# Kernel optimization log

Measured on AMD Instinct MI355X. Metric: run time of the kernel, lower is better.

The kernel has to match this reference:

```python
import jax, jax.numpy as jnp
import numpy as np
import math

B, S, D, H = 2, 4096, 512, 8
DK = D // H


def setup_inputs() -> dict:
    key = jax.random.key(0)
    ks = jax.random.split(key, 9)
    s = 1.0 / math.sqrt(D)
    return {
        "x": jax.random.normal(ks[0], (B, S, D), dtype=jnp.float32),
        "Wq": jax.random.normal(ks[1], (D, D), dtype=jnp.float32) * s,
        "bq": jax.random.normal(ks[2], (D,), dtype=jnp.float32) * 0.01,
        "Wk": jax.random.normal(ks[3], (D, D), dtype=jnp.float32) * s,
        "bk": jax.random.normal(ks[4], (D,), dtype=jnp.float32) * 0.01,
        "Wv": jax.random.normal(ks[5], (D, D), dtype=jnp.float32) * s,
        "bv": jax.random.normal(ks[6], (D,), dtype=jnp.float32) * 0.01,
        "Wo": jax.random.normal(ks[7], (D, D), dtype=jnp.float32) * s,
        "bo": jax.random.normal(ks[8], (D,), dtype=jnp.float32) * 0.01,
    }


def reference(x, Wq, bq, Wk, bk, Wv, bv, Wo, bo):
    b, s, _ = x.shape
    # projections, split into heads: (b, h, s, dk)
    def proj(W, bias):
        return (x @ W.T + bias).reshape(b, s, H, DK).transpose(0, 2, 1, 3)
    Q, K, V = proj(Wq, bq), proj(Wk, bk), proj(Wv, bv)
    scale = 1.0 / math.sqrt(DK)
    scores = jnp.einsum("bhqd,bhkd->bhqk", Q, K) * scale  # (b,h,s,s)
    causal = jnp.tril(jnp.ones((s, s), dtype=bool))
    scores = jnp.where(causal[None, None], scores, -jnp.inf)
    attn = jax.nn.softmax(scores, axis=-1)
    out = jnp.einsum("bhqk,bhkd->bhqd", attn, V)
    out = out.transpose(0, 2, 1, 3).reshape(b, s, D)
    return out @ Wo.T + bo
```

## Files before the change

kernel.cpp:

```cpp
#include <hip/hip_runtime.h>
#include <hip/hip_bf16.h>

using u16    = unsigned short;
using u32    = unsigned int;
using bf16x8 = __attribute__((ext_vector_type(8))) __bf16;
using s16x4  = __attribute__((ext_vector_type(4))) short;
using f32x4  = __attribute__((ext_vector_type(4))) float;
using u16x4  = __attribute__((ext_vector_type(4))) unsigned short;
using u16x8  = __attribute__((ext_vector_type(8))) unsigned short;
using u32x2  = __attribute__((ext_vector_type(2))) unsigned int;
using u32x4  = __attribute__((ext_vector_type(4))) unsigned int;


static __device__ __forceinline__ u16 f2bf(float f) {
  unsigned int u = __float_as_uint(f);
  u += 0x7fffu + ((u >> 16) & 1u);
  return (u16)(u >> 16);
}
static __device__ __forceinline__ u32 pack2bf(float lo, float hi) {
  return __builtin_amdgcn_perm(__float_as_uint(hi), __float_as_uint(lo), 0x07060302u);
}

__global__ __launch_bounds__(256) void cvt_all(
    const float* __restrict__ x,  const float* __restrict__ wq,
    const float* __restrict__ wk, const float* __restrict__ wv,
    const float* __restrict__ wo,
    u16* __restrict__ xb, u16* __restrict__ wqb, u16* __restrict__ wkb,
    u16* __restrict__ wvb, u16* __restrict__ wob) {
  const int bx = blockIdx.x;
  const float* src;
  u16* dst;
  int i;
  if (bx < 4096) {
    src = x; dst = xb; i = bx * 256 + threadIdx.x;
  } else {
    const int t  = (bx - 4096) >> 8;
    const int lb = (bx - 4096) & 255;
    src = (t == 0) ? wq : (t == 1) ? wk : (t == 2) ? wv : wo;
    dst = (t == 0) ? wqb : (t == 1) ? wkb : (t == 2) ? wvb : wob;
    i = lb * 256 + threadIdx.x;
  }
  float4 v = reinterpret_cast<const float4*>(src)[i];
  u16x4 o = { f2bf(v.x), f2bf(v.y), f2bf(v.z), f2bf(v.w) };
  reinterpret_cast<u16x4*>(dst)[i] = o;
}

__global__ __launch_bounds__(256, 3) void gemm_qkv(const u16* __restrict__ A,
                                                   const u16* __restrict__ Wq,
                                                   const u16* __restrict__ Wk,
                                                   const u16* __restrict__ Wv,
                                                   const float* __restrict__ bqp,
                                                   const float* __restrict__ bkp,
                                                   const float* __restrict__ bvp,
                                                   u16* __restrict__ Qo,
                                                   u16* __restrict__ Ko,
                                                   u16* __restrict__ Vto) {
  const int which = blockIdx.z;
  const u16* W = (which == 0) ? Wq : (which == 1) ? Wk : Wv;
  const float* bias = (which == 0) ? bqp : (which == 1) ? bkp : bvp;

  __shared__ u16 sA[128 * 72];
  __shared__ u16 sB[128 * 72];
  const int row0 = blockIdx.x * 128;
  const int col0 = blockIdx.y * 128;
  const int tid  = threadIdx.x;
  const int lane = tid & 63;
  const int wave = tid >> 6;
  const int wm   = (wave & 1) * 64;
  const int wn   = (wave >> 1) * 64;
  const int ln   = lane & 15;
  const int quad = lane >> 4;

  int rr[4], cc[4];
  for (int i = 0; i < 4; ++i) {
    const int idx = tid + 256 * i;
    rr[i] = idx >> 3; cc[i] = (idx & 7) * 8;
  }

  f32x4 zero = {0.f, 0.f, 0.f, 0.f};
  f32x4 acc[4][4];
  for (int i = 0; i < 4; ++i)
    for (int j = 0; j < 4; ++j) acc[i][j] = zero;

  u16x8 curA[4], nxtA[4];
  for (int i = 0; i < 4; ++i)
    curA[i] = *reinterpret_cast<const u16x8*>(&A[(row0 + rr[i]) * 512 + cc[i]]);

  for (int k0 = 0; k0 < 512; k0 += 64) {
    __syncthreads();
    for (int i = 0; i < 4; ++i) {
      *reinterpret_cast<u16x8*>(&sA[rr[i] * 72 + cc[i]]) = curA[i];
      *reinterpret_cast<u16x8*>(&sB[rr[i] * 72 + cc[i]]) =
          *reinterpret_cast<const u16x8*>(&W[(col0 + rr[i]) * 512 + k0 + cc[i]]);
    }
    if (k0 < 448)
      for (int i = 0; i < 4; ++i)
        nxtA[i] = *reinterpret_cast<const u16x8*>(&A[(row0 + rr[i]) * 512 + k0 + 64 + cc[i]]);
    __syncthreads();
    for (int ks = 0; ks < 2; ++ks) {
      bf16x8 af[4], bfr[4];
      for (int t4 = 0; t4 < 4; ++t4)
        af[t4] = *reinterpret_cast<const bf16x8*>(&sA[(wm + t4 * 16 + ln) * 72 + ks * 32 + quad * 8]);
      for (int t4 = 0; t4 < 4; ++t4)
        bfr[t4] = *reinterpret_cast<const bf16x8*>(&sB[(wn + t4 * 16 + ln) * 72 + ks * 32 + quad * 8]);
      for (int tm = 0; tm < 4; ++tm)
        for (int tn = 0; tn < 4; ++tn)
          acc[tm][tn] = __builtin_amdgcn_mfma_f32_16x16x32_bf16(af[tm], bfr[tn], acc[tm][tn], 0, 0, 0);
    }
    for (int i = 0; i < 4; ++i) curA[i] = nxtA[i];
  }

  if (which < 2) {
    u16* out = (which == 0) ? Qo : Ko;
    const float scale = (which == 0) ? 0.125f : 1.0f;
    for (int tm = 0; tm < 4; ++tm) {
      const int mbase = row0 + wm + tm * 16 + quad * 4;
      for (int tn = 0; tn < 4; ++tn) {
        const int n  = col0 + wn + tn * 16 + ln;
        const int h  = n >> 6, dk = n & 63;
        const float bv = bias[n];
        for (int r = 0; r < 4; ++r) {
          const int m  = mbase + r;
          const int bh = ((m >> 12) << 3) + h;
          const int s  = m & 4095;
          out[(bh * 4096 + s) * 64 + dk] = f2bf((acc[tm][tn][r] + bv) * scale);
        }
      }
    }
  } else {
    for (int tm = 0; tm < 4; ++tm) {
      const int mbase = row0 + wm + tm * 16 + quad * 4;
      const int b_idx = mbase >> 12;
      const int s     = mbase & 4095;
      for (int tn = 0; tn < 4; ++tn) {
        const int n  = col0 + wn + tn * 16 + ln;
        const int h  = n >> 6, dk = n & 63;
        const int bh = b_idx * 8 + h;
        const float bv = bias[n];
        u16x4 o;
        for (int r = 0; r < 4; ++r) o[r] = f2bf(acc[tm][tn][r] + bv);
        *reinterpret_cast<u16x4*>(&Vto[(bh * 64 + dk) * 4096 + s]) = o;
      }
    }
  }
}

__global__ __launch_bounds__(256, 3) void gemm_out(const u16* __restrict__ A,
                                                   const u16* __restrict__ W,
                                                   const float* __restrict__ bias,
                                                   float* __restrict__ out) {
  __shared__ u16 sA[128 * 72];
  __shared__ u16 sB[128 * 72];
  const int row0 = blockIdx.x * 128;
  const int col0 = blockIdx.y * 128;
  const int tid  = threadIdx.x;
  const int lane = tid & 63;
  const int wave = tid >> 6;
  const int wm   = (wave & 1) * 64;
  const int wn   = (wave >> 1) * 64;
  const int ln   = lane & 15;
  const int quad = lane >> 4;

  int rr[4], cc[4];
  for (int i = 0; i < 4; ++i) {
    const int idx = tid + 256 * i;
    rr[i] = idx >> 3; cc[i] = (idx & 7) * 8;
  }

  f32x4 zero = {0.f, 0.f, 0.f, 0.f};
  f32x4 acc[4][4];
  for (int i = 0; i < 4; ++i)
    for (int j = 0; j < 4; ++j) acc[i][j] = zero;

  u16x8 curA[4], nxtA[4];
  for (int i = 0; i < 4; ++i)
    curA[i] = *reinterpret_cast<const u16x8*>(&A[(row0 + rr[i]) * 512 + cc[i]]);

  for (int k0 = 0; k0 < 512; k0 += 64) {
    __syncthreads();
    for (int i = 0; i < 4; ++i) {
      *reinterpret_cast<u16x8*>(&sA[rr[i] * 72 + cc[i]]) = curA[i];
      *reinterpret_cast<u16x8*>(&sB[rr[i] * 72 + cc[i]]) =
          *reinterpret_cast<const u16x8*>(&W[(col0 + rr[i]) * 512 + k0 + cc[i]]);
    }
    if (k0 < 448)
      for (int i = 0; i < 4; ++i)
        nxtA[i] = *reinterpret_cast<const u16x8*>(&A[(row0 + rr[i]) * 512 + k0 + 64 + cc[i]]);
    __syncthreads();
    for (int ks = 0; ks < 2; ++ks) {
      bf16x8 af[4], bfr[4];
      for (int t4 = 0; t4 < 4; ++t4)
        af[t4] = *reinterpret_cast<const bf16x8*>(&sA[(wm + t4 * 16 + ln) * 72 + ks * 32 + quad * 8]);
      for (int t4 = 0; t4 < 4; ++t4)
        bfr[t4] = *reinterpret_cast<const bf16x8*>(&sB[(wn + t4 * 16 + ln) * 72 + ks * 32 + quad * 8]);
      for (int tm = 0; tm < 4; ++tm)
        for (int tn = 0; tn < 4; ++tn)
          acc[tm][tn] = __builtin_amdgcn_mfma_f32_16x16x32_bf16(af[tm], bfr[tn], acc[tm][tn], 0, 0, 0);
    }
    for (int i = 0; i < 4; ++i) curA[i] = nxtA[i];
  }

  for (int tm = 0; tm < 4; ++tm) {
    const int mbase = row0 + wm + tm * 16 + quad * 4;
    for (int tn = 0; tn < 4; ++tn) {
      const int n  = col0 + wn + tn * 16 + ln;
      const float bv = bias[n];
      for (int r = 0; r < 4; ++r)
        out[(mbase + r) * 512 + n] = acc[tm][tn][r] + bv;
    }
  }
}

#if __has_builtin(__builtin_amdgcn_mfma_f32_16x16x16bf16_1k)
#define HAVE_MFMA16 1
#endif
__global__ __launch_bounds__(256, 4) void attn_part(const u16* __restrict__ Q,
                                                    const u16* __restrict__ K,
                                                    const u16* __restrict__ Vt,
                                                    float* __restrict__ pO,
                                                    float* __restrict__ pl) {
  const int c = blockIdx.x;
  const int t = blockIdx.y;
  const int ga = t >> 3;
  if (c > ga) return;
  const int ktlast = 2 * t + 1;
  const int kt0 = 16 * c;
  const int kt1 = (kt0 + 15 < ktlast) ? (kt0 + 15) : ktlast;
  const int bh = blockIdx.z;
  const int qb = t * 128;

  const u16* Qh  = Q  + bh * 4096 * 64;
  const u16* Kh  = K  + bh * 4096 * 64;
  const u16* Vth = Vt + bh * 64 * 4096;

  __shared__ u16 sK[64 * 72];
  __shared__ u16 sV[64 * 72];

  const int tid  = threadIdx.x;
  const int lane = tid & 63;
  const int wave = tid >> 6;
  const int ln   = lane & 15;
  const int quad = lane >> 4;

  const int r0 = tid >> 3,         c0 = (tid & 7) * 8;
  const int r1 = (tid + 256) >> 3, c1 = ((tid + 256) & 7) * 8;

  bf16x8 qf[2][2];
  for (int tn = 0; tn < 2; ++tn)
    for (int ks = 0; ks < 2; ++ks)
      qf[tn][ks] = *reinterpret_cast<const bf16x8*>(
          &Qh[(qb + wave * 32 + tn * 16 + ln) * 64 + ks * 32 + quad * 8]);

  f32x4 zero = {0.f, 0.f, 0.f, 0.f};
  f32x4 accO[4][2];
  float lsum[2] = {0.f, 0.f};
  for (int td = 0; td < 4; ++td)
    for (int tn = 0; tn < 2; ++tn) accO[td][tn] = zero;

#ifndef HAVE_MFMA16
  const int idx0 = 4 * (ln + 16 * (2 * (quad & 1)));
#endif

  u16x8 cur[4], nxt[4];
  {
    const int kb = kt0 * 64;
    cur[0] = *reinterpret_cast<const u16x8*>(&Kh[(kb + r0) * 64 + c0]);
    cur[1] = *reinterpret_cast<const u16x8*>(&Kh[(kb + r1) * 64 + c1]);
    cur[2] = *reinterpret_cast<const u16x8*>(&Vth[r0 * 4096 + kb + c0]);
    cur[3] = *reinterpret_cast<const u16x8*>(&Vth[r1 * 4096 + kb + c1]);
  }

  for (int kt = kt0; kt <= kt1; ++kt) {
    const int kb = kt * 64;
    __syncthreads();
    *reinterpret_cast<u16x8*>(&sK[r0 * 72 + c0]) = cur[0];
    *reinterpret_cast<u16x8*>(&sK[r1 * 72 + c1]) = cur[1];
    *reinterpret_cast<u16x8*>(&sV[r0 * 72 + c0]) = cur[2];
    *reinterpret_cast<u16x8*>(&sV[r1 * 72 + c1]) = cur[3];
    if (kt < kt1) {
      const int kn = kb + 64;
      nxt[0] = *reinterpret_cast<const u16x8*>(&Kh[(kn + r0) * 64 + c0]);
      nxt[1] = *reinterpret_cast<const u16x8*>(&Kh[(kn + r1) * 64 + c1]);
      nxt[2] = *reinterpret_cast<const u16x8*>(&Vth[r0 * 4096 + kn + c0]);
      nxt[3] = *reinterpret_cast<const u16x8*>(&Vth[r1 * 4096 + kn + c1]);
    }
    __syncthreads();

    f32x4 accS[4][2];
    for (int tm = 0; tm < 4; ++tm)
      for (int tn = 0; tn < 2; ++tn) accS[tm][tn] = zero;
    for (int tm = 0; tm < 4; ++tm) {
      bf16x8 kf0 = *reinterpret_cast<const bf16x8*>(&sK[(tm * 16 + ln) * 72 + quad * 8]);
      bf16x8 kf1 = *reinterpret_cast<const bf16x8*>(&sK[(tm * 16 + ln) * 72 + 32 + quad * 8]);
      for (int tn = 0; tn < 2; ++tn) {
        accS[tm][tn] = __builtin_amdgcn_mfma_f32_16x16x32_bf16(kf0, qf[tn][0], accS[tm][tn], 0, 0, 0);
        accS[tm][tn] = __builtin_amdgcn_mfma_f32_16x16x32_bf16(kf1, qf[tn][1], accS[tm][tn], 0, 0, 0);
      }
    }

    const bool diag = (kt >= 2 * t);
    u32 pp[4][2][2];
    for (int tm = 0; tm < 4; ++tm)
      for (int tn = 0; tn < 2; ++tn) {
        f32x4 e = accS[tm][tn];
        if (diag) {
          const int kg = kb + tm * 16 + quad * 4;
          const int qg = qb + wave * 32 + tn * 16 + ln;
          for (int r = 0; r < 4; ++r)
            if (kg + r > qg) e[r] = -__builtin_inff();
        }
        for (int r = 0; r < 4; ++r) e[r] = __expf(e[r]);
        lsum[tn] += (e[0] + e[1]) + (e[2] + e[3]);
        pp[tm][tn][0] = pack2bf(e[0], e[1]);
        pp[tm][tn][1] = pack2bf(e[2], e[3]);
      }

#ifdef HAVE_MFMA16
    for (int k16 = 0; k16 < 4; ++k16)
      for (int td = 0; td < 4; ++td) {
        s16x4 vf = *reinterpret_cast<const s16x4*>(&sV[(td * 16 + ln) * 72 + k16 * 16 + quad * 4]);
        for (int tn = 0; tn < 2; ++tn) {
          u32x2 pr = { pp[k16][tn][0], pp[k16][tn][1] };
          s16x4 pb = __builtin_bit_cast(s16x4, pr);
          accO[td][tn] = __builtin_amdgcn_mfma_f32_16x16x16bf16_1k(vf, pb, accO[td][tn], 0, 0, 0);
        }
      }
#else
    for (int ks = 0; ks < 2; ++ks)
      for (int tn = 0; tn < 2; ++tn) {
        u32 b[4];
        for (int half = 0; half < 2; ++half)
          for (int p = 0; p < 2; ++p) {
            int v0 = __builtin_amdgcn_ds_bpermute(idx0 + 64 * half, (int)pp[2 * ks][tn][p]);
            int v1 = __builtin_amdgcn_ds_bpermute(idx0 + 64 * half, (int)pp[2 * ks + 1][tn][p]);
            b[half * 2 + p] = (quad < 2) ? (u32)v0 : (u32)v1;
          }
        u32x4 bv4 = { b[0], b[1], b[2], b[3] };
        bf16x8 pfrag = __builtin_bit_cast(bf16x8, bv4);
        for (int td = 0; td < 4; ++td) {
          bf16x8 vf = *reinterpret_cast<const bf16x8*>(&sV[(td * 16 + ln) * 72 + ks * 32 + quad * 8]);
          accO[td][tn] = __builtin_amdgcn_mfma_f32_16x16x32_bf16(vf, pfrag, accO[td][tn], 0, 0, 0);
        }
      }
#endif
    for (int j = 0; j < 4; ++j) cur[j] = nxt[j];
  }

  for (int tn = 0; tn < 2; ++tn) {
    lsum[tn] += __shfl_xor(lsum[tn], 16);
    lsum[tn] += __shfl_xor(lsum[tn], 32);
  }
  const int slot = bh * 80 + t + 4 * ga * (ga - 1) + ga * (t & 7) + c;
  float* po = pO + (size_t)slot * 8192;
  for (int td = 0; td < 4; ++td)
    for (int tn = 0; tn < 2; ++tn)
      for (int r = 0; r < 4; ++r)
        po[(td * 16 + quad * 4 + r) * 128 + wave * 32 + tn * 16 + ln] = accO[td][tn][r];
  if (quad == 0)
    for (int tn = 0; tn < 2; ++tn)
      pl[slot * 128 + wave * 32 + tn * 16 + ln] = lsum[tn];
}

__global__ __launch_bounds__(256) void attn_comb(const float* __restrict__ pO,
                                                 const float* __restrict__ pl,
                                                 u16* __restrict__ ctx) {
  const int t  = blockIdx.x;
  const int bh = blockIdx.y;
  const int ga = t >> 3;
  const int nch = ga + 1;
  const int base = bh * 80 + t + 4 * ga * (ga - 1) + ga * (t & 7);
  const int tid = threadIdx.x;

  __shared__ float sO[64 * 132];
  __shared__ float sL[128];

  float4 acc[8];
  for (int i = 0; i < 8; ++i) acc[i] = make_float4(0.f, 0.f, 0.f, 0.f);
  float lacc = 0.f;
  for (int cidx = 0; cidx < nch; ++cidx) {
    const float* src = pO + (size_t)(base + cidx) * 8192;
    for (int i = 0; i < 8; ++i) {
      float4 v = reinterpret_cast<const float4*>(src)[i * 256 + tid];
      acc[i].x += v.x; acc[i].y += v.y; acc[i].z += v.z; acc[i].w += v.w;
    }
    if (tid < 128) lacc += pl[(base + cidx) * 128 + tid];
  }
  for (int i = 0; i < 8; ++i) {
    const int f = i * 256 + tid;
    const int d = f >> 5, q = (f & 31) * 4;
    *reinterpret_cast<float4*>(&sO[d * 132 + q]) = acc[i];
  }
  if (tid < 128) sL[tid] = lacc;
  __syncthreads();

  const int q  = tid >> 1;
  const int d0 = (tid & 1) * 32;
  const float inv = 1.0f / sL[q];
  const int b_idx = bh >> 3, h = bh & 7;
  const int tok = (b_idx << 12) + t * 128 + q;
  u16* dst = &ctx[tok * 512 + h * 64 + d0];
  for (int g = 0; g < 4; ++g) {
    u16x8 ov;
    for (int j = 0; j < 8; ++j) ov[j] = f2bf(sO[(d0 + g * 8 + j) * 132 + q] * inv);
    *reinterpret_cast<u16x8*>(&dst[g * 8]) = ov;
  }
}

extern "C" void kernel_launch(void* const* d_in, const int* in_sizes, int n_in,
                              void* d_out, int out_size, void* d_ws, size_t ws_size,
                              hipStream_t stream) {
  const float* x  = (const float*)d_in[0];
  const float* Wq = (const float*)d_in[1];
  const float* bq = (const float*)d_in[2];
  const float* Wk = (const float*)d_in[3];
  const float* bk = (const float*)d_in[4];
  const float* Wv = (const float*)d_in[5];
  const float* bv = (const float*)d_in[6];
  const float* Wo = (const float*)d_in[7];
  const float* bo = (const float*)d_in[8];
  float* out = (float*)d_out;

  char* ws = (char*)d_ws;
  u16* xb  = (u16*)(ws + 0);
  u16* wqb = (u16*)(ws + 8388608);
  u16* wkb = (u16*)(ws + 8912896);
  u16* wvb = (u16*)(ws + 9437184);
  u16* wob = (u16*)(ws + 9961472);
  u16* Qb  = (u16*)(ws + 10485760);
  u16* Kb  = (u16*)(ws + 18874368);
  u16* Vtb = (u16*)(ws + 27262976);
  float* pO = (float*)(ws + 35651584);
  float* pl = (float*)(ws + 77594624);
  u16* ctx = xb;

  cvt_all<<<5120, 256, 0, stream>>>(x, Wq, Wk, Wv, Wo, xb, wqb, wkb, wvb, wob);
  gemm_qkv<<<dim3(64, 4, 3), 256, 0, stream>>>(xb, wqb, wkb, wvb, bq, bk, bv, Qb, Kb, Vtb);
  attn_part<<<dim3(4, 32, 16), 256, 0, stream>>>(Qb, Kb, Vtb, pO, pl);
  attn_comb<<<dim3(32, 16), 256, 0, stream>>>(pO, pl, ctx);
  gemm_out<<<dim3(64, 4), 256, 0, stream>>>(ctx, wob, bo, out);
}
```

Before: 209.2 us.

## Prefetch weight tiles in GEMMs, balance attention split-K chunks, add MFMA priority

The two projection GEMMs now register-prefetch the W tile one step ahead, like the A tile, and move the barrier so next-tile global loads are issued after the LDS store barrier and overlap the MFMA work. The attention kernel splits each query tile's key range evenly across its chunks instead of using fixed 16-tile chunks, which balances per-block work across the causal triangle. It also moves the barrier before the prefetch loads and wraps MFMA sections in s_setprio to favour matrix issue. The cost is extra registers for the B prefetch, which may reduce occupancy.

```diff
diff --git a/kernel.cpp b/kernel.cpp
--- a/kernel.cpp
+++ b/kernel.cpp
@@ -82,21 +82,24 @@
   for (int i = 0; i < 4; ++i)
     for (int j = 0; j < 4; ++j) acc[i][j] = zero;
 
-  u16x8 curA[4], nxtA[4];
-  for (int i = 0; i < 4; ++i)
+  u16x8 curA[4], nxtA[4], curB[4], nxtB[4];
+  for (int i = 0; i < 4; ++i) {
     curA[i] = *reinterpret_cast<const u16x8*>(&A[(row0 + rr[i]) * 512 + cc[i]]);
+    curB[i] = *reinterpret_cast<const u16x8*>(&W[(col0 + rr[i]) * 512 + cc[i]]);
+  }
 
   for (int k0 = 0; k0 < 512; k0 += 64) {
     __syncthreads();
     for (int i = 0; i < 4; ++i) {
       *reinterpret_cast<u16x8*>(&sA[rr[i] * 72 + cc[i]]) = curA[i];
-      *reinterpret_cast<u16x8*>(&sB[rr[i] * 72 + cc[i]]) =
-          *reinterpret_cast<const u16x8*>(&W[(col0 + rr[i]) * 512 + k0 + cc[i]]);
-    }
+      *reinterpret_cast<u16x8*>(&sB[rr[i] * 72 + cc[i]]) = curB[i];
+    }
+    __syncthreads();
     if (k0 < 448)
-      for (int i = 0; i < 4; ++i)
+      for (int i = 0; i < 4; ++i) {
         nxtA[i] = *reinterpret_cast<const u16x8*>(&A[(row0 + rr[i]) * 512 + k0 + 64 + cc[i]]);
-    __syncthreads();
+        nxtB[i] = *reinterpret_cast<const u16x8*>(&W[(col0 + rr[i]) * 512 + k0 + 64 + cc[i]]);
+      }
     for (int ks = 0; ks < 2; ++ks) {
       bf16x8 af[4], bfr[4];
       for (int t4 = 0; t4 < 4; ++t4)
@@ -107,7 +110,7 @@
         for (int tn = 0; tn < 4; ++tn)
           acc[tm][tn] = __builtin_amdgcn_mfma_f32_16x16x32_bf16(af[tm], bfr[tn], acc[tm][tn], 0, 0, 0);
     }
-    for (int i = 0; i < 4; ++i) curA[i] = nxtA[i];
+    for (int i = 0; i < 4; ++i) { curA[i] = nxtA[i]; curB[i] = nxtB[i]; }
   }
 
   if (which < 2) {
@@ -172,21 +175,24 @@
   for (int i = 0; i < 4; ++i)
     for (int j = 0; j < 4; ++j) acc[i][j] = zero;
 
-  u16x8 curA[4], nxtA[4];
-  for (int i = 0; i < 4; ++i)
+  u16x8 curA[4], nxtA[4], curB[4], nxtB[4];
+  for (int i = 0; i < 4; ++i) {
     curA[i] = *reinterpret_cast<const u16x8*>(&A[(row0 + rr[i]) * 512 + cc[i]]);
+    curB[i] = *reinterpret_cast<const u16x8*>(&W[(col0 + rr[i]) * 512 + cc[i]]);
+  }
 
   for (int k0 = 0; k0 < 512; k0 += 64) {
     __syncthreads();
     for (int i = 0; i < 4; ++i) {
       *reinterpret_cast<u16x8*>(&sA[rr[i] * 72 + cc[i]]) = curA[i];
-      *reinterpret_cast<u16x8*>(&sB[rr[i] * 72 + cc[i]]) =
-          *reinterpret_cast<const u16x8*>(&W[(col0 + rr[i]) * 512 + k0 + cc[i]]);
-    }
+      *reinterpret_cast<u16x8*>(&sB[rr[i] * 72 + cc[i]]) = curB[i];
+    }
+    __syncthreads();
     if (k0 < 448)
-      for (int i = 0; i < 4; ++i)
+      for (int i = 0; i < 4; ++i) {
         nxtA[i] = *reinterpret_cast<const u16x8*>(&A[(row0 + rr[i]) * 512 + k0 + 64 + cc[i]]);
-    __syncthreads();
+        nxtB[i] = *reinterpret_cast<const u16x8*>(&W[(col0 + rr[i]) * 512 + k0 + 64 + cc[i]]);
+      }
     for (int ks = 0; ks < 2; ++ks) {
       bf16x8 af[4], bfr[4];
       for (int t4 = 0; t4 < 4; ++t4)
@@ -197,7 +203,7 @@
         for (int tn = 0; tn < 4; ++tn)
           acc[tm][tn] = __builtin_amdgcn_mfma_f32_16x16x32_bf16(af[tm], bfr[tn], acc[tm][tn], 0, 0, 0);
     }
-    for (int i = 0; i < 4; ++i) curA[i] = nxtA[i];
+    for (int i = 0; i < 4; ++i) { curA[i] = nxtA[i]; curB[i] = nxtB[i]; }
   }
 
   for (int tm = 0; tm < 4; ++tm) {
@@ -222,10 +228,13 @@
   const int c = blockIdx.x;
   const int t = blockIdx.y;
   const int ga = t >> 3;
-  if (c > ga) return;
-  const int ktlast = 2 * t + 1;
-  const int kt0 = 16 * c;
-  const int kt1 = (kt0 + 15 < ktlast) ? (kt0 + 15) : ktlast;
+  const int nch = ga + 1;
+  if (c >= nch) return;
+  const int ntiles = 2 * t + 2;
+  const int len = (ntiles + nch - 1) / nch;
+  const int kt0 = c * len;
+  const int kt1e = kt0 + len;
+  const int kt1 = ((kt1e < ntiles) ? kt1e : ntiles) - 1;
   const int bh = blockIdx.z;
   const int qb = t * 128;
 
@@ -277,6 +286,7 @@
     *reinterpret_cast<u16x8*>(&sK[r1 * 72 + c1]) = cur[1];
     *reinterpret_cast<u16x8*>(&sV[r0 * 72 + c0]) = cur[2];
     *reinterpret_cast<u16x8*>(&sV[r1 * 72 + c1]) = cur[3];
+    __syncthreads();
     if (kt < kt1) {
       const int kn = kb + 64;
       nxt[0] = *reinterpret_cast<const u16x8*>(&Kh[(kn + r0) * 64 + c0]);
@@ -284,11 +294,11 @@
       nxt[2] = *reinterpret_cast<const u16x8*>(&Vth[r0 * 4096 + kn + c0]);
       nxt[3] = *reinterpret_cast<const u16x8*>(&Vth[r1 * 4096 + kn + c1]);
     }
-    __syncthreads();
 
     f32x4 accS[4][2];
     for (int tm = 0; tm < 4; ++tm)
       for (int tn = 0; tn < 2; ++tn) accS[tm][tn] = zero;
+    __builtin_amdgcn_s_setprio(1);
     for (int tm = 0; tm < 4; ++tm) {
       bf16x8 kf0 = *reinterpret_cast<const bf16x8*>(&sK[(tm * 16 + ln) * 72 + quad * 8]);
       bf16x8 kf1 = *reinterpret_cast<const bf16x8*>(&sK[(tm * 16 + ln) * 72 + 32 + quad * 8]);
@@ -297,6 +307,7 @@
         accS[tm][tn] = __builtin_amdgcn_mfma_f32_16x16x32_bf16(kf1, qf[tn][1], accS[tm][tn], 0, 0, 0);
       }
     }
+    __builtin_amdgcn_s_setprio(0);
 
     const bool diag = (kt >= 2 * t);
     u32 pp[4][2][2];
@@ -316,6 +327,7 @@
       }
 
 #ifdef HAVE_MFMA16
+    __builtin_amdgcn_s_setprio(1);
     for (int k16 = 0; k16 < 4; ++k16)
       for (int td = 0; td < 4; ++td) {
         s16x4 vf = *reinterpret_cast<const s16x4*>(&sV[(td * 16 + ln) * 72 + k16 * 16 + quad * 4]);
@@ -325,6 +337,7 @@
           accO[td][tn] = __builtin_amdgcn_mfma_f32_16x16x16bf16_1k(vf, pb, accO[td][tn], 0, 0, 0);
         }
       }
+    __builtin_amdgcn_s_setprio(0);
 #else
     for (int ks = 0; ks < 2; ++ks)
       for (int tn = 0; tn < 2; ++tn) {
@@ -337,10 +350,12 @@
           }
         u32x4 bv4 = { b[0], b[1], b[2], b[3] };
         bf16x8 pfrag = __builtin_bit_cast(bf16x8, bv4);
+        __builtin_amdgcn_s_setprio(1);
         for (int td = 0; td < 4; ++td) {
           bf16x8 vf = *reinterpret_cast<const bf16x8*>(&sV[(td * 16 + ln) * 72 + ks * 32 + quad * 8]);
           accO[td][tn] = __builtin_amdgcn_mfma_f32_16x16x32_bf16(vf, pfrag, accO[td][tn], 0, 0, 0);
         }
+        __builtin_amdgcn_s_setprio(0);
       }
 #endif
     for (int j = 0; j < 4; ++j) cur[j] = nxt[j];
```

Result: faster. 203.4 us (-2.8%).
